# Kernel optimization log

Hardware: AMD Instinct MI355X
Metric: run time of the kernel (lower is better)

Reference implementation:

```python
import jax, jax.numpy as jnp
import numpy as np
import math

N_NODES = 100000
N_EDGES = 1600000
IN_FEATS = 64
H_FEATS = 64
NUM_CLASSES = 2
LS_D = [2, 4, 6, 8]
LS_COEFF = [1.0, 1.0, 1.0, 1.0]
K = 4  # polynomial order per conv (len of each theta)


def _chi_theta(d, coeff):
    # Faithful port of calculate_theta_Chi for d > 0: fit chi-square-like
    # density on [0,2] with a degree-3 Chebyshev series, reverse coeffs.
    n = 2 * d
    m = 1.0 / (n / 2 + 1)  # i = n/2 - 1, m = 1/(i+2)
    def y(x):
        x = np.asarray(x, dtype=np.float64)
        return 1.0 / (2 ** (n / 2) * math.gamma(n / 2)) * (x / m) ** (n / 2 - 1) * np.exp(-(x / m) / 2)
    xs = np.linspace(0.0, 2.0, 20001)
    S = np.trapz(y(xs), xs)  # dense trapezoid ~ scipy.integrate.quad on [0,2]
    lambs = np.linspace(0.0, 2.0, 500)
    c = np.polynomial.chebyshev.chebfit(lambs, y(lambs) / S, 3)
    return (c[::-1] * coeff).astype(np.float32)

THETAS_NP = np.stack([_chi_theta(d, c) for d, c in zip(LS_D, LS_COEFF)])  # [4, K]


def setup_inputs() -> dict:
    key = jax.random.key(0)
    ks = jax.random.split(key, 8)
    sc = 0.05
    return {
        "x": jax.random.normal(ks[0], (N_NODES, IN_FEATS), dtype=jnp.float32),
        "src": jax.random.randint(ks[1], (N_EDGES,), 0, N_NODES, dtype=jnp.int32),
        "dst": jax.random.randint(ks[2], (N_EDGES,), 0, N_NODES, dtype=jnp.int32),
        "thetas": jnp.asarray(THETAS_NP),
        "W1": jax.random.normal(ks[3], (IN_FEATS, H_FEATS), dtype=jnp.float32) * sc,
        "b1": jnp.zeros((H_FEATS,), dtype=jnp.float32),
        "W2": jax.random.normal(ks[4], (H_FEATS, H_FEATS), dtype=jnp.float32) * sc,
        "b2": jnp.zeros((H_FEATS,), dtype=jnp.float32),
        "Wm1": jax.random.normal(ks[5], (H_FEATS * len(LS_D), H_FEATS), dtype=jnp.float32) * sc,
        "bm1": jnp.zeros((H_FEATS,), dtype=jnp.float32),
        "Wm2": jax.random.normal(ks[6], (H_FEATS, NUM_CLASSES), dtype=jnp.float32) * sc,
        "bm2": jnp.zeros((NUM_CLASSES,), dtype=jnp.float32),
    }


def reference(x, src, dst, thetas, W1, b1, W2, b2, Wm1, bm1, Wm2, bm2):
    n = x.shape[0]
    # input MLP stem
    h = jax.nn.relu(x @ W1 + b1)
    h = jax.nn.relu(h @ W2 + b2)
    # D^{-1/2} from in-degrees (clamped to >= 1), as in DGL in_degrees()
    deg = jax.ops.segment_sum(jnp.ones_like(dst, dtype=h.dtype), dst, num_segments=n)
    dinv = jnp.maximum(deg, 1.0) ** -0.5  # [N]
    dinv = dinv[:, None]  # [N, 1]
    # shared Laplacian power sequence: feats[k] = L^k h with L = I - D^-1/2 A D^-1/2
    feats = [h]
    f = h
    for _ in range(K - 1):
        t = f * dinv                                   # [N, H]
        agg = jax.ops.segment_sum(t[src], dst, num_segments=n)  # gather-scatter SpMM
        f = f - agg * dinv
        feats.append(f)
    F = jnp.stack(feats)  # [K, N, H]
    # per-conv polynomial combination, then concat along feature dim
    h_final = jnp.einsum('ck,knh->nch', thetas, F).reshape(n, -1)  # [N, C*H]
    # output MLP (2 layers)
    h_out = jax.nn.relu(h_final @ Wm1 + bm1)
    return h_out @ Wm2 + bm2
```

## Files before the change

kernel.cpp:

```cpp
#include <hip/hip_runtime.h>
#include <math.h>

#define FS3 192
#define TS  256
#define BCAP2 4608
#define CHUNK 4096

typedef __attribute__((ext_vector_type(8))) short short8v;
typedef __attribute__((ext_vector_type(4))) float f32x4;

__device__ __forceinline__ unsigned short f2bf(float f) {
    unsigned int u = __builtin_bit_cast(unsigned int, f);
    u += 0x7fff + ((u >> 16) & 1);
    return (unsigned short)(u >> 16);
}
__device__ __forceinline__ float bf2f(unsigned short s) {
    return __builtin_bit_cast(float, ((unsigned int)s) << 16);
}
__device__ __forceinline__ void fma4(float4& a, float s, const float4& b) {
    a.x = fmaf(s, b.x, a.x);
    a.y = fmaf(s, b.y, a.y);
    a.z = fmaf(s, b.z, a.z);
    a.w = fmaf(s, b.w, a.w);
}

__global__ void zero_k(int* __restrict__ p, int n) {
    int i = blockIdx.x * blockDim.x + threadIdx.x;
    int st = gridDim.x * blockDim.x;
    for (; i < n; i += st) p[i] = 0;
}

__global__ __launch_bounds__(256) void part1_k(const int* __restrict__ src,
        const int* __restrict__ dst, int* __restrict__ gcnt,
        unsigned int* __restrict__ pairs, int E, int NB) {
    __shared__ int lcnt[512];
    __shared__ int lbase[512];
    __shared__ int lpos[512];
    int tid = threadIdx.x;
    int base = blockIdx.x * CHUNK;
    int m = E - base; if (m > CHUNK) m = CHUNK;
    for (int b = tid; b < NB; b += 256) { lcnt[b] = 0; lpos[b] = 0; }
    __syncthreads();
    for (int i = tid; i < m; i += 256)
        atomicAdd(&lcnt[dst[base + i] >> 8], 1);
    __syncthreads();
    for (int b = tid; b < NB; b += 256)
        lbase[b] = (lcnt[b] > 0) ? atomicAdd(&gcnt[b], lcnt[b]) : 0;
    __syncthreads();
    for (int i = tid; i < m; i += 256) {
        int s = src[base + i], d = dst[base + i];
        int b = d >> 8;
        int p = atomicAdd(&lpos[b], 1);
        int idx = lbase[b] + p;
        if (idx < BCAP2)
            pairs[(size_t)b * BCAP2 + idx] = (unsigned int)s | ((unsigned int)(d & 255) << 17);
    }
}

__global__ __launch_bounds__(512) void bscan_k(const int* __restrict__ gcnt,
        int* __restrict__ bbase, int* __restrict__ rowp, int NB, int E, int n) {
    __shared__ int buf[512];
    int tid = threadIdx.x;
    int v = (tid < NB) ? (gcnt[tid] > BCAP2 ? BCAP2 : gcnt[tid]) : 0;
    buf[tid] = v;
    __syncthreads();
    int x = v;
    for (int off = 1; off < 512; off <<= 1) {
        int t = (tid >= off) ? buf[tid - off] : 0;
        __syncthreads();
        x += t;
        buf[tid] = x;
        __syncthreads();
    }
    if (tid < NB) bbase[tid] = x - v;
    if (tid == 0) rowp[n] = E;
}

__global__ __launch_bounds__(256) void csr2_k(const int* __restrict__ gcnt,
        const unsigned int* __restrict__ pairs, const int* __restrict__ bbase,
        int* __restrict__ rowp, int* __restrict__ colb, float* __restrict__ dinv, int n) {
    int b = blockIdx.x;
    int tid = threadIdx.x;
    int cntb = gcnt[b]; if (cntb > BCAP2) cntb = BCAP2;
    const unsigned int* pb = pairs + (size_t)b * BCAP2;
    __shared__ int c[256];
    __shared__ int sc[256];
    __shared__ int lpos[256];
    c[tid] = 0; lpos[tid] = 0;
    __syncthreads();
    for (int i = tid; i < cntb; i += 256)
        atomicAdd(&c[pb[i] >> 17], 1);
    __syncthreads();
    int v = c[tid];
    sc[tid] = v;
    __syncthreads();
    int x = v;
    for (int off = 1; off < 256; off <<= 1) {
        int t = (tid >= off) ? sc[tid - off] : 0;
        __syncthreads();
        x += t;
        sc[tid] = x;
        __syncthreads();
    }
    int ex = x - v;
    sc[tid] = ex;
    int node = b * 256 + tid;
    if (node < n) {
        rowp[node] = bbase[b] + ex;
        dinv[node] = 1.0f / sqrtf((float)(v > 1 ? v : 1));
    }
    __syncthreads();
    for (int i = tid; i < cntb; i += 256) {
        unsigned int pk = pb[i];
        int j = pk >> 17;
        int p = atomicAdd(&lpos[j], 1);
        colb[bbase[b] + sc[j] + p] = (int)(pk & 0x1FFFF);
    }
}

__global__ __launch_bounds__(256) void mlp_k(const float* __restrict__ x,
        const float* __restrict__ W1, const float* __restrict__ b1,
        const float* __restrict__ W2, const float* __restrict__ b2,
        const float* __restrict__ dinv,
        float* __restrict__ F, unsigned short* __restrict__ Tcat, int n, int ntiles) {
    __shared__ float Ws1[64 * 64];
    __shared__ float Ws2[64 * 64];
    __shared__ float xT[64 * 68];
    int tid = threadIdx.x;
    int ti = tid >> 4, tj = tid & 15;
    for (int idx = tid; idx < 4096; idx += 256) { Ws1[idx] = W1[idx]; Ws2[idx] = W2[idx]; }
    float4 b1v = *(const float4*)&b1[4 * tj];
    float4 b2v = *(const float4*)&b2[4 * tj];

    for (int g = blockIdx.x; g < ntiles; g += gridDim.x) {
        int base = g * 64;
        __syncthreads();
        for (int it = 0; it < 4; it++) {
            int node = ti + it * 16;
            int gn = base + node;
            float4 v = make_float4(0.f, 0.f, 0.f, 0.f);
            if (gn < n) v = *(const float4*)&x[(size_t)gn * 64 + 4 * tj];
            xT[(4 * tj + 0) * 68 + node] = v.x;
            xT[(4 * tj + 1) * 68 + node] = v.y;
            xT[(4 * tj + 2) * 68 + node] = v.z;
            xT[(4 * tj + 3) * 68 + node] = v.w;
        }
        __syncthreads();

        float4 a0 = b1v, a1 = b1v, a2 = b1v, a3 = b1v;
        #pragma unroll 8
        for (int k = 0; k < 64; k++) {
            float4 xv = *(const float4*)&xT[k * 68 + 4 * ti];
            float4 wv = *(const float4*)&Ws1[k * 64 + 4 * tj];
            fma4(a0, xv.x, wv); fma4(a1, xv.y, wv); fma4(a2, xv.z, wv); fma4(a3, xv.w, wv);
        }
        __syncthreads();
        {
            int hb = (4 * tj) * 68 + 4 * ti;
            xT[hb + 0 * 68 + 0] = fmaxf(a0.x, 0.f);
            xT[hb + 1 * 68 + 0] = fmaxf(a0.y, 0.f);
            xT[hb + 2 * 68 + 0] = fmaxf(a0.z, 0.f);
            xT[hb + 3 * 68 + 0] = fmaxf(a0.w, 0.f);
            xT[hb + 0 * 68 + 1] = fmaxf(a1.x, 0.f);
            xT[hb + 1 * 68 + 1] = fmaxf(a1.y, 0.f);
            xT[hb + 2 * 68 + 1] = fmaxf(a1.z, 0.f);
            xT[hb + 3 * 68 + 1] = fmaxf(a1.w, 0.f);
            xT[hb + 0 * 68 + 2] = fmaxf(a2.x, 0.f);
            xT[hb + 1 * 68 + 2] = fmaxf(a2.y, 0.f);
            xT[hb + 2 * 68 + 2] = fmaxf(a2.z, 0.f);
            xT[hb + 3 * 68 + 2] = fmaxf(a2.w, 0.f);
            xT[hb + 0 * 68 + 3] = fmaxf(a3.x, 0.f);
            xT[hb + 1 * 68 + 3] = fmaxf(a3.y, 0.f);
            xT[hb + 2 * 68 + 3] = fmaxf(a3.z, 0.f);
            xT[hb + 3 * 68 + 3] = fmaxf(a3.w, 0.f);
        }
        __syncthreads();

        a0 = b2v; a1 = b2v; a2 = b2v; a3 = b2v;
        #pragma unroll 8
        for (int k = 0; k < 64; k++) {
            float4 xv = *(const float4*)&xT[k * 68 + 4 * ti];
            float4 wv = *(const float4*)&Ws2[k * 64 + 4 * tj];
            fma4(a0, xv.x, wv); fma4(a1, xv.y, wv); fma4(a2, xv.z, wv); fma4(a3, xv.w, wv);
        }
        int gn0 = base + 4 * ti;
#define STORE_ROW(ai, ii)                                                                  \
        {                                                                                  \
            int gn = gn0 + (ii);                                                           \
            if (gn < n) {                                                                  \
                float r0 = fmaxf(ai.x, 0.f), r1 = fmaxf(ai.y, 0.f);                        \
                float r2 = fmaxf(ai.z, 0.f), r3 = fmaxf(ai.w, 0.f);                        \
                *(float4*)&F[(size_t)gn * FS3 + 4 * tj] = make_float4(r0, r1, r2, r3);     \
                float dg = dinv[gn];                                                       \
                ushort4 tv;                                                                \
                tv.x = f2bf(r0 * dg); tv.y = f2bf(r1 * dg);                                \
                tv.z = f2bf(r2 * dg); tv.w = f2bf(r3 * dg);                                \
                *(ushort4*)&Tcat[(size_t)gn * TS + 4 * tj] = tv;                           \
            }                                                                              \
        }
        STORE_ROW(a0, 0) STORE_ROW(a1, 1) STORE_ROW(a2, 2) STORE_ROW(a3, 3)
#undef STORE_ROW
    }
}

__global__ void wm1p_k(const float* __restrict__ thetas, const float* __restrict__ Wm1,
                       unsigned short* __restrict__ Wth, unsigned short* __restrict__ Wtl) {
    int idx = blockIdx.x * blockDim.x + threadIdx.x;
    if (idx >= 16384) return;
    int j = idx & 63;
    int q = idx >> 6;
    int k = q >> 6;
    int hh = q & 63;
    float a = 0.f;
    for (int c = 0; c < 4; c++) a += thetas[c * 4 + k] * Wm1[(c * 64 + hh) * 64 + j];
    unsigned short hi = f2bf(a);
    float r = a - bf2f(hi);
    Wth[j * 256 + q] = hi;
    Wtl[j * 256 + q] = f2bf(r);
}

__global__ __launch_bounds__(256) void prop_k(const float* __restrict__ Fin,
        float* __restrict__ Fout,
        const unsigned short* __restrict__ Tin, unsigned short* __restrict__ Tout,
        const int* __restrict__ rowp, const int* __restrict__ colb,
        const float* __restrict__ dinv, int n, int writeF) {
    int w = (blockIdx.x * blockDim.x + threadIdx.x) >> 6;
    int lane = threadIdx.x & 63;
    int nA = 2 * w, nB = 2 * w + 1;
    if (nA >= n) return;
    bool hasB = (nB < n);
    int eA = rowp[nA], endA = rowp[nA + 1];
    int eB = 0, endB = 0;
    if (hasB) { eB = rowp[nB]; endB = rowp[nB + 1]; }
    float a0 = 0.f, a1 = 0.f, b0 = 0.f, b1 = 0.f;
    while (eA + 3 < endA && eB + 3 < endB) {
        int sA0 = colb[eA], sA1 = colb[eA + 1], sA2 = colb[eA + 2], sA3 = colb[eA + 3];
        int sB0 = colb[eB], sB1 = colb[eB + 1], sB2 = colb[eB + 2], sB3 = colb[eB + 3];
        float fA0 = bf2f(Tin[(size_t)sA0 * TS + lane]);
        float fA1 = bf2f(Tin[(size_t)sA1 * TS + lane]);
        float fA2 = bf2f(Tin[(size_t)sA2 * TS + lane]);
        float fA3 = bf2f(Tin[(size_t)sA3 * TS + lane]);
        float fB0 = bf2f(Tin[(size_t)sB0 * TS + lane]);
        float fB1 = bf2f(Tin[(size_t)sB1 * TS + lane]);
        float fB2 = bf2f(Tin[(size_t)sB2 * TS + lane]);
        float fB3 = bf2f(Tin[(size_t)sB3 * TS + lane]);
        a0 += fA0 + fA2; a1 += fA1 + fA3;
        b0 += fB0 + fB2; b1 += fB1 + fB3;
        eA += 4; eB += 4;
    }
    while (eA + 3 < endA) {
        int s0 = colb[eA], s1 = colb[eA + 1], s2 = colb[eA + 2], s3 = colb[eA + 3];
        float f0 = bf2f(Tin[(size_t)s0 * TS + lane]);
        float f1 = bf2f(Tin[(size_t)s1 * TS + lane]);
        float f2 = bf2f(Tin[(size_t)s2 * TS + lane]);
        float f3 = bf2f(Tin[(size_t)s3 * TS + lane]);
        a0 += f0 + f2; a1 += f1 + f3;
        eA += 4;
    }
    while (eB + 3 < endB) {
        int s0 = colb[eB], s1 = colb[eB + 1], s2 = colb[eB + 2], s3 = colb[eB + 3];
        float f0 = bf2f(Tin[(size_t)s0 * TS + lane]);
        float f1 = bf2f(Tin[(size_t)s1 * TS + lane]);
        float f2 = bf2f(Tin[(size_t)s2 * TS + lane]);
        float f3 = bf2f(Tin[(size_t)s3 * TS + lane]);
        b0 += f0 + f2; b1 += f1 + f3;
        eB += 4;
    }
    for (; eA < endA; ++eA) a0 += bf2f(Tin[(size_t)colb[eA] * TS + lane]);
    for (; eB < endB; ++eB) b0 += bf2f(Tin[(size_t)colb[eB] * TS + lane]);

    {
        float acc = a0 + a1;
        float dg = dinv[nA];
        float fo = Fin[(size_t)nA * FS3 + lane] - acc * dg;
        if (writeF) Fout[(size_t)nA * FS3 + lane] = fo;
        Tout[(size_t)nA * TS + lane] = f2bf(fo * dg);
    }
    if (hasB) {
        float acc = b0 + b1;
        float dg = dinv[nB];
        float fo = Fin[(size_t)nB * FS3 + lane] - acc * dg;
        if (writeF) Fout[(size_t)nB * FS3 + lane] = fo;
        Tout[(size_t)nB * TS + lane] = f2bf(fo * dg);
    }
}

__global__ __launch_bounds__(512, 4) void final_k(const unsigned short* __restrict__ Tcat,
        const float* __restrict__ dinv,
        const unsigned short* __restrict__ Wth, const unsigned short* __restrict__ Wtl,
        const float* __restrict__ bm1, const float* __restrict__ Wm2,
        const float* __restrict__ bm2, float* __restrict__ out, int n) {
    __shared__ float Lp[4][128][2];
    int tid = threadIdx.x;
    int w = tid >> 6, l = tid & 63;
    int cw = w & 3, half = w >> 2;
    int colg = 16 * cw + (l & 15);
    int krow = (l >> 4) * 8;

    short8v bhi[8], blo[8];
    #pragma unroll
    for (int ks = 0; ks < 8; ks++) {
        bhi[ks] = *(const short8v*)&Wth[colg * 256 + ks * 32 + krow];
        blo[ks] = *(const short8v*)&Wtl[colg * 256 + ks * 32 + krow];
    }
    float bm1c = bm1[colg];
    float w2x = Wm2[colg * 2 + 0], w2y = Wm2[colg * 2 + 1];

    int gbase = blockIdx.x * 128 + half * 64;
    const unsigned short* abase = &Tcat[(size_t)(gbase + (l & 15)) * TS + krow];

    for (int rt = 0; rt < 4; rt++) {
        f32x4 acc = {0.f, 0.f, 0.f, 0.f};
        const unsigned short* ap = abase + (size_t)rt * 16 * TS;
        #pragma unroll
        for (int ks = 0; ks < 8; ks++) {
            short8v a = *(const short8v*)(ap + ks * 32);
            acc = __builtin_amdgcn_mfma_f32_16x16x32_bf16(a, bhi[ks], acc, 0, 0, 0);
            acc = __builtin_amdgcn_mfma_f32_16x16x32_bf16(a, blo[ks], acc, 0, 0, 0);
        }
        #pragma unroll
        for (int i = 0; i < 4; i++) {
            int rl = half * 64 + rt * 16 + (l >> 4) * 4 + i;
            int grow = blockIdx.x * 128 + rl;
            float s = (grow < n) ? (1.0f / dinv[grow]) : 0.f;
            float h = fmaxf(fmaf(acc[i], s, bm1c), 0.f);
            float q0 = h * w2x, q1 = h * w2y;
            q0 += __shfl_xor(q0, 1); q1 += __shfl_xor(q1, 1);
            q0 += __shfl_xor(q0, 2); q1 += __shfl_xor(q1, 2);
            q0 += __shfl_xor(q0, 4); q1 += __shfl_xor(q1, 4);
            q0 += __shfl_xor(q0, 8); q1 += __shfl_xor(q1, 8);
            if ((l & 15) == 0) {
                Lp[cw][rl][0] = q0;
                Lp[cw][rl][1] = q1;
            }
        }
    }
    __syncthreads();
    if (tid < 256) {
        int r = tid >> 1, ch = tid & 1;
        int grow = blockIdx.x * 128 + r;
        if (grow < n) {
            float v = Lp[0][r][ch] + Lp[1][r][ch] + Lp[2][r][ch] + Lp[3][r][ch] + bm2[ch];
            out[grow * 2 + ch] = v;
        }
    }
}

extern "C" void kernel_launch(void* const* d_in, const int* in_sizes, int n_in,
                              void* d_out, int out_size, void* d_ws, size_t ws_size,
                              hipStream_t stream) {
    const float* x      = (const float*)d_in[0];
    const int*   src    = (const int*)d_in[1];
    const int*   dst    = (const int*)d_in[2];
    const float* thetas = (const float*)d_in[3];
    const float* W1     = (const float*)d_in[4];
    const float* b1     = (const float*)d_in[5];
    const float* W2     = (const float*)d_in[6];
    const float* b2     = (const float*)d_in[7];
    const float* Wm1    = (const float*)d_in[8];
    const float* bm1    = (const float*)d_in[9];
    const float* Wm2    = (const float*)d_in[10];
    const float* bm2    = (const float*)d_in[11];
    float* out = (float*)d_out;

    int n = in_sizes[0] / 64;
    int E = in_sizes[1];
    int ntiles  = (n + 63) / 64;
    int ntiles2 = (n + 127) / 128;
    int NB = (n + 255) / 256;

    float* Fbuf  = (float*)d_ws;
    float* dinv  = Fbuf + (size_t)n * FS3;
    int*   rowp  = (int*)(dinv + n);
    int*   colb  = rowp + (n + 1);
    size_t woff = (((size_t)(colb + E) - (size_t)d_ws) + 15) & ~(size_t)15;
    unsigned short* Wth = (unsigned short*)((char*)d_ws + woff);
    unsigned short* Wtl = Wth + 16384;
    int*   gcnt  = (int*)(Wtl + 16384);
    int*   bbase = gcnt + NB;
    size_t uoff = (((size_t)(bbase + NB) - (size_t)d_ws) + 255) & ~(size_t)255;
    unsigned int*   pairs = (unsigned int*)((char*)d_ws + uoff);
    unsigned short* Tcat  = (unsigned short*)pairs;

    int nchunksP = (E + CHUNK - 1) / CHUNK;

    zero_k<<<4, 256, 0, stream>>>(gcnt, NB);
    part1_k<<<nchunksP, 256, 0, stream>>>(src, dst, gcnt, pairs, E, NB);
    bscan_k<<<1, 512, 0, stream>>>(gcnt, bbase, rowp, NB, E, n);
    csr2_k<<<NB, 256, 0, stream>>>(gcnt, pairs, bbase, rowp, colb, dinv, n);

    mlp_k<<<768, 256, 0, stream>>>(x, W1, b1, W2, b2, dinv, Fbuf, Tcat, n, ntiles);
    wm1p_k<<<64, 256, 0, stream>>>(thetas, Wm1, Wth, Wtl);

    int nwaves = (n + 1) / 2;
    int pblocks = ((size_t)nwaves * 64 + 255) / 256;
    prop_k<<<pblocks, 256, 0, stream>>>(
        Fbuf + 0 * 64, Fbuf + 1 * 64, Tcat + 0 * 64, Tcat + 1 * 64, rowp, colb, dinv, n, 1);
    prop_k<<<pblocks, 256, 0, stream>>>(
        Fbuf + 1 * 64, Fbuf + 2 * 64, Tcat + 1 * 64, Tcat + 2 * 64, rowp, colb, dinv, n, 1);
    prop_k<<<pblocks, 256, 0, stream>>>(
        Fbuf + 2 * 64, Fbuf + 2 * 64, Tcat + 2 * 64, Tcat + 3 * 64, rowp, colb, dinv, n, 0);

    final_k<<<ntiles2, 512, 0, stream>>>(Tcat, dinv, Wth, Wtl, bm1, Wm2, bm2, out, n);
}
```

Baseline: 295.2 us.

## Replace fp32 residual feature buffer with bf16 hi/lo split of scaled features

```diff
diff --git a/kernel.cpp b/kernel.cpp
--- a/kernel.cpp
+++ b/kernel.cpp
@@ -1,8 +1,8 @@
 #include <hip/hip_runtime.h>
 #include <math.h>
 
-#define FS3 192
 #define TS  256
+#define GS  192
 #define BCAP2 4608
 #define CHUNK 4096
 
@@ -122,7 +122,8 @@
         const float* __restrict__ W1, const float* __restrict__ b1,
         const float* __restrict__ W2, const float* __restrict__ b2,
         const float* __restrict__ dinv,
-        float* __restrict__ F, unsigned short* __restrict__ Tcat, int n, int ntiles) {
+        unsigned short* __restrict__ Ghi, unsigned short* __restrict__ Glo,
+        int n, int ntiles) {
     __shared__ float Ws1[64 * 64];
     __shared__ float Ws2[64 * 64];
     __shared__ float xT[64 * 68];
@@ -188,14 +189,16 @@
         {                                                                                  \
             int gn = gn0 + (ii);                                                           \
             if (gn < n) {                                                                  \
-                float r0 = fmaxf(ai.x, 0.f), r1 = fmaxf(ai.y, 0.f);                        \
-                float r2 = fmaxf(ai.z, 0.f), r3 = fmaxf(ai.w, 0.f);                        \
-                *(float4*)&F[(size_t)gn * FS3 + 4 * tj] = make_float4(r0, r1, r2, r3);     \
                 float dg = dinv[gn];                                                       \
-                ushort4 tv;                                                                \
-                tv.x = f2bf(r0 * dg); tv.y = f2bf(r1 * dg);                                \
-                tv.z = f2bf(r2 * dg); tv.w = f2bf(r3 * dg);                                \
-                *(ushort4*)&Tcat[(size_t)gn * TS + 4 * tj] = tv;                           \
+                float g0 = fmaxf(ai.x, 0.f) * dg, g1 = fmaxf(ai.y, 0.f) * dg;              \
+                float g2 = fmaxf(ai.z, 0.f) * dg, g3 = fmaxf(ai.w, 0.f) * dg;              \
+                ushort4 hv, lv;                                                            \
+                hv.x = f2bf(g0); lv.x = f2bf(g0 - bf2f(hv.x));                             \
+                hv.y = f2bf(g1); lv.y = f2bf(g1 - bf2f(hv.y));                             \
+                hv.z = f2bf(g2); lv.z = f2bf(g2 - bf2f(hv.z));                             \
+                hv.w = f2bf(g3); lv.w = f2bf(g3 - bf2f(hv.w));                             \
+                *(ushort4*)&Ghi[(size_t)gn * TS + 4 * tj] = hv;                            \
+                *(ushort4*)&Glo[(size_t)gn * GS + 4 * tj] = lv;                            \
             }                                                                              \
         }
         STORE_ROW(a0, 0) STORE_ROW(a1, 1) STORE_ROW(a2, 2) STORE_ROW(a3, 3)
@@ -219,11 +222,13 @@
     Wtl[j * 256 + q] = f2bf(r);
 }
 
-__global__ __launch_bounds__(256) void prop_k(const float* __restrict__ Fin,
-        float* __restrict__ Fout,
-        const unsigned short* __restrict__ Tin, unsigned short* __restrict__ Tout,
+__global__ __launch_bounds__(256) void prop_k(
+        const unsigned short* __restrict__ TinHi,
+        const unsigned short* __restrict__ TinLo,
+        unsigned short* __restrict__ ToutHi,
+        unsigned short* __restrict__ ToutLo,
         const int* __restrict__ rowp, const int* __restrict__ colb,
-        const float* __restrict__ dinv, int n, int writeF) {
+        const float* __restrict__ dinv, int n, int writeLo) {
     int w = (blockIdx.x * blockDim.x + threadIdx.x) >> 6;
     int lane = threadIdx.x & 63;
     int nA = 2 * w, nB = 2 * w + 1;
@@ -233,55 +238,93 @@
     int eB = 0, endB = 0;
     if (hasB) { eB = rowp[nB]; endB = rowp[nB + 1]; }
     float a0 = 0.f, a1 = 0.f, b0 = 0.f, b1 = 0.f;
-    while (eA + 3 < endA && eB + 3 < endB) {
-        int sA0 = colb[eA], sA1 = colb[eA + 1], sA2 = colb[eA + 2], sA3 = colb[eA + 3];
-        int sB0 = colb[eB], sB1 = colb[eB + 1], sB2 = colb[eB + 2], sB3 = colb[eB + 3];
-        float fA0 = bf2f(Tin[(size_t)sA0 * TS + lane]);
-        float fA1 = bf2f(Tin[(size_t)sA1 * TS + lane]);
-        float fA2 = bf2f(Tin[(size_t)sA2 * TS + lane]);
-        float fA3 = bf2f(Tin[(size_t)sA3 * TS + lane]);
-        float fB0 = bf2f(Tin[(size_t)sB0 * TS + lane]);
-        float fB1 = bf2f(Tin[(size_t)sB1 * TS + lane]);
-        float fB2 = bf2f(Tin[(size_t)sB2 * TS + lane]);
-        float fB3 = bf2f(Tin[(size_t)sB3 * TS + lane]);
-        a0 += fA0 + fA2; a1 += fA1 + fA3;
-        b0 += fB0 + fB2; b1 += fB1 + fB3;
-        eA += 4; eB += 4;
+    while (eA + 7 < endA && eB + 7 < endB) {
+        int sA0 = __builtin_nontemporal_load(&colb[eA]);
+        int sA1 = __builtin_nontemporal_load(&colb[eA + 1]);
+        int sA2 = __builtin_nontemporal_load(&colb[eA + 2]);
+        int sA3 = __builtin_nontemporal_load(&colb[eA + 3]);
+        int sA4 = __builtin_nontemporal_load(&colb[eA + 4]);
+        int sA5 = __builtin_nontemporal_load(&colb[eA + 5]);
+        int sA6 = __builtin_nontemporal_load(&colb[eA + 6]);
+        int sA7 = __builtin_nontemporal_load(&colb[eA + 7]);
+        int sB0 = __builtin_nontemporal_load(&colb[eB]);
+        int sB1 = __builtin_nontemporal_load(&colb[eB + 1]);
+        int sB2 = __builtin_nontemporal_load(&colb[eB + 2]);
+        int sB3 = __builtin_nontemporal_load(&colb[eB + 3]);
+        int sB4 = __builtin_nontemporal_load(&colb[eB + 4]);
+        int sB5 = __builtin_nontemporal_load(&colb[eB + 5]);
+        int sB6 = __builtin_nontemporal_load(&colb[eB + 6]);
+        int sB7 = __builtin_nontemporal_load(&colb[eB + 7]);
+        float fA0 = bf2f(TinHi[(size_t)sA0 * TS + lane]);
+        float fA1 = bf2f(TinHi[(size_t)sA1 * TS + lane]);
+        float fA2 = bf2f(TinHi[(size_t)sA2 * TS + lane]);
+        float fA3 = bf2f(TinHi[(size_t)sA3 * TS + lane]);
+        float fA4 = bf2f(TinHi[(size_t)sA4 * TS + lane]);
+        float fA5 = bf2f(TinHi[(size_t)sA5 * TS + lane]);
+        float fA6 = bf2f(TinHi[(size_t)sA6 * TS + lane]);
+        float fA7 = bf2f(TinHi[(size_t)sA7 * TS + lane]);
+        float fB0 = bf2f(TinHi[(size_t)sB0 * TS + lane]);
+        float fB1 = bf2f(TinHi[(size_t)sB1 * TS + lane]);
+        float fB2 = bf2f(TinHi[(size_t)sB2 * TS + lane]);
+        float fB3 = bf2f(TinHi[(size_t)sB3 * TS + lane]);
+        float fB4 = bf2f(TinHi[(size_t)sB4 * TS + lane]);
+        float fB5 = bf2f(TinHi[(size_t)sB5 * TS + lane]);
+        float fB6 = bf2f(TinHi[(size_t)sB6 * TS + lane]);
+        float fB7 = bf2f(TinHi[(size_t)sB7 * TS + lane]);
+        a0 += (fA0 + fA2) + (fA4 + fA6);
+        a1 += (fA1 + fA3) + (fA5 + fA7);
+        b0 += (fB0 + fB2) + (fB4 + fB6);
+        b1 += (fB1 + fB3) + (fB5 + fB7);
+        eA += 8; eB += 8;
     }
     while (eA + 3 < endA) {
-        int s0 = colb[eA], s1 = colb[eA + 1], s2 = colb[eA + 2], s3 = colb[eA + 3];
-        float f0 = bf2f(Tin[(size_t)s0 * TS + lane]);
-        float f1 = bf2f(Tin[(size_t)s1 * TS + lane]);
-        float f2 = bf2f(Tin[(size_t)s2 * TS + lane]);
-        float f3 = bf2f(Tin[(size_t)s3 * TS + lane]);
+        int s0 = __builtin_nontemporal_load(&colb[eA]);
+        int s1 = __builtin_nontemporal_load(&colb[eA + 1]);
+        int s2 = __builtin_nontemporal_load(&colb[eA + 2]);
+        int s3 = __builtin_nontemporal_load(&colb[eA + 3]);
+        float f0 = bf2f(TinHi[(size_t)s0 * TS + lane]);
+        float f1 = bf2f(TinHi[(size_t)s1 * TS + lane]);
+        float f2 = bf2f(TinHi[(size_t)s2 * TS + lane]);
+        float f3 = bf2f(TinHi[(size_t)s3 * TS + lane]);
         a0 += f0 + f2; a1 += f1 + f3;
         eA += 4;
     }
     while (eB + 3 < endB) {
-        int s0 = colb[eB], s1 = colb[eB + 1], s2 = colb[eB + 2], s3 = colb[eB + 3];
-        float f0 = bf2f(Tin[(size_t)s0 * TS + lane]);
-        float f1 = bf2f(Tin[(size_t)s1 * TS + lane]);
-        float f2 = bf2f(Tin[(size_t)s2 * TS + lane]);
-        float f3 = bf2f(Tin[(size_t)s3 * TS + lane]);
+        int s0 = __builtin_nontemporal_load(&colb[eB]);
+        int s1 = __builtin_nontemporal_load(&colb[eB + 1]);
+        int s2 = __builtin_nontemporal_load(&colb[eB + 2]);
+        int s3 = __builtin_nontemporal_load(&colb[eB + 3]);
+        float f0 = bf2f(TinHi[(size_t)s0 * TS + lane]);
+        float f1 = bf2f(TinHi[(size_t)s1 * TS + lane]);
+        float f2 = bf2f(TinHi[(size_t)s2 * TS + lane]);
+        float f3 = bf2f(TinHi[(size_t)s3 * TS + lane]);
         b0 += f0 + f2; b1 += f1 + f3;
         eB += 4;
     }
-    for (; eA < endA; ++eA) a0 += bf2f(Tin[(size_t)colb[eA] * TS + lane]);
-    for (; eB < endB; ++eB) b0 += bf2f(Tin[(size_t)colb[eB] * TS + lane]);
+    for (; eA < endA; ++eA) a0 += bf2f(TinHi[(size_t)__builtin_nontemporal_load(&colb[eA]) * TS + lane]);
+    for (; eB < endB; ++eB) b0 += bf2f(TinHi[(size_t)__builtin_nontemporal_load(&colb[eB]) * TS + lane]);
 
     {
         float acc = a0 + a1;
         float dg = dinv[nA];
-        float fo = Fin[(size_t)nA * FS3 + lane] - acc * dg;
-        if (writeF) Fout[(size_t)nA * FS3 + lane] = fo;
-        Tout[(size_t)nA * TS + lane] = f2bf(fo * dg);
+        float gin = bf2f(__builtin_nontemporal_load(&TinHi[(size_t)nA * TS + lane]))
+                  + bf2f(__builtin_nontemporal_load(&TinLo[(size_t)nA * GS + lane]));
+        float go = gin - dg * dg * acc;
+        unsigned short hi = f2bf(go);
+        ToutHi[(size_t)nA * TS + lane] = hi;
+        if (writeLo)
+            __builtin_nontemporal_store(f2bf(go - bf2f(hi)), &ToutLo[(size_t)nA * GS + lane]);
     }
     if (hasB) {
         float acc = b0 + b1;
         float dg = dinv[nB];
-        float fo = Fin[(size_t)nB * FS3 + lane] - acc * dg;
-        if (writeF) Fout[(size_t)nB * FS3 + lane] = fo;
-        Tout[(size_t)nB * TS + lane] = f2bf(fo * dg);
+        float gin = bf2f(__builtin_nontemporal_load(&TinHi[(size_t)nB * TS + lane]))
+                  + bf2f(__builtin_nontemporal_load(&TinLo[(size_t)nB * GS + lane]));
+        float go = gin - dg * dg * acc;
+        unsigned short hi = f2bf(go);
+        ToutHi[(size_t)nB * TS + lane] = hi;
+        if (writeLo)
+            __builtin_nontemporal_store(f2bf(go - bf2f(hi)), &ToutLo[(size_t)nB * GS + lane]);
     }
 }
 
@@ -369,8 +412,8 @@
     int ntiles2 = (n + 127) / 128;
     int NB = (n + 255) / 256;
 
-    float* Fbuf  = (float*)d_ws;
-    float* dinv  = Fbuf + (size_t)n * FS3;
+    unsigned short* Glo = (unsigned short*)d_ws;
+    float* dinv  = (float*)(Glo + (size_t)n * GS);
     int*   rowp  = (int*)(dinv + n);
     int*   colb  = rowp + (n + 1);
     size_t woff = (((size_t)(colb + E) - (size_t)d_ws) + 15) & ~(size_t)15;
@@ -380,7 +423,7 @@
     int*   bbase = gcnt + NB;
     size_t uoff = (((size_t)(bbase + NB) - (size_t)d_ws) + 255) & ~(size_t)255;
     unsigned int*   pairs = (unsigned int*)((char*)d_ws + uoff);
-    unsigned short* Tcat  = (unsigned short*)pairs;
+    unsigned short* Ghi   = (unsigned short*)pairs;
 
     int nchunksP = (E + CHUNK - 1) / CHUNK;
 
@@ -389,17 +432,17 @@
     bscan_k<<<1, 512, 0, stream>>>(gcnt, bbase, rowp, NB, E, n);
     csr2_k<<<NB, 256, 0, stream>>>(gcnt, pairs, bbase, rowp, colb, dinv, n);
 
-    mlp_k<<<768, 256, 0, stream>>>(x, W1, b1, W2, b2, dinv, Fbuf, Tcat, n, ntiles);
+    mlp_k<<<768, 256, 0, stream>>>(x, W1, b1, W2, b2, dinv, Ghi, Glo, n, ntiles);
     wm1p_k<<<64, 256, 0, stream>>>(thetas, Wm1, Wth, Wtl);
 
     int nwaves = (n + 1) / 2;
     int pblocks = ((size_t)nwaves * 64 + 255) / 256;
     prop_k<<<pblocks, 256, 0, stream>>>(
-        Fbuf + 0 * 64, Fbuf + 1 * 64, Tcat + 0 * 64, Tcat + 1 * 64, rowp, colb, dinv, n, 1);
+        Ghi + 0 * 64, Glo + 0 * 64, Ghi + 1 * 64, Glo + 1 * 64, rowp, colb, dinv, n, 1);
     prop_k<<<pblocks, 256, 0, stream>>>(
-        Fbuf + 1 * 64, Fbuf + 2 * 64, Tcat + 1 * 64, Tcat + 2 * 64, rowp, colb, dinv, n, 1);
+        Ghi + 1 * 64, Glo + 1 * 64, Ghi + 2 * 64, Glo + 2 * 64, rowp, colb, dinv, n, 1);
     prop_k<<<pblocks, 256, 0, stream>>>(
-        Fbuf + 2 * 64, Fbuf + 2 * 64, Tcat + 2 * 64, Tcat + 3 * 64, rowp, colb, dinv, n, 0);
-
-    final_k<<<ntiles2, 512, 0, stream>>>(Tcat, dinv, Wth, Wtl, bm1, Wm2, bm2, out, n);
-}
+        Ghi + 2 * 64, Glo + 2 * 64, Ghi + 3 * 64, Glo + 2 * 64, rowp, colb, dinv, n, 0);
+
+    final_k<<<ntiles2, 512, 0, stream>>>(Ghi, dinv, Wth, Wtl, bm1, Wm2, bm2, out, n);
+}
```

After: 341.2 us. 15.6% more time.

## Store propagated features as 8-column bf16 hi/lo slabs for cache-local gathers

Applied to the files above, without the earlier changes.

```diff
diff --git a/kernel.cpp b/kernel.cpp
--- a/kernel.cpp
+++ b/kernel.cpp
@@ -1,13 +1,13 @@
 #include <hip/hip_runtime.h>
 #include <math.h>
 
-#define FS3 192
-#define TS  256
 #define BCAP2 4608
 #define CHUNK 4096
+#define NPB 256
 
 typedef __attribute__((ext_vector_type(8))) short short8v;
 typedef __attribute__((ext_vector_type(4))) float f32x4;
+
 
 __device__ __forceinline__ unsigned short f2bf(float f) {
     unsigned int u = __builtin_bit_cast(unsigned int, f);
@@ -122,7 +122,8 @@
         const float* __restrict__ W1, const float* __restrict__ b1,
         const float* __restrict__ W2, const float* __restrict__ b2,
         const float* __restrict__ dinv,
-        float* __restrict__ F, unsigned short* __restrict__ Tcat, int n, int ntiles) {
+        unsigned short* __restrict__ Ghi, unsigned short* __restrict__ Glo,
+        int n, int ntiles, size_t npad8) {
     __shared__ float Ws1[64 * 64];
     __shared__ float Ws2[64 * 64];
     __shared__ float xT[64 * 68];
@@ -131,6 +132,8 @@
     for (int idx = tid; idx < 4096; idx += 256) { Ws1[idx] = W1[idx]; Ws2[idx] = W2[idx]; }
     float4 b1v = *(const float4*)&b1[4 * tj];
     float4 b2v = *(const float4*)&b2[4 * tj];
+    int kb = tj >> 1;
+    int off = (tj & 1) * 4;
 
     for (int g = blockIdx.x; g < ntiles; g += gridDim.x) {
         int base = g * 64;
@@ -188,14 +191,16 @@
         {                                                                                  \
             int gn = gn0 + (ii);                                                           \
             if (gn < n) {                                                                  \
-                float r0 = fmaxf(ai.x, 0.f), r1 = fmaxf(ai.y, 0.f);                        \
-                float r2 = fmaxf(ai.z, 0.f), r3 = fmaxf(ai.w, 0.f);                        \
-                *(float4*)&F[(size_t)gn * FS3 + 4 * tj] = make_float4(r0, r1, r2, r3);     \
                 float dg = dinv[gn];                                                       \
-                ushort4 tv;                                                                \
-                tv.x = f2bf(r0 * dg); tv.y = f2bf(r1 * dg);                                \
-                tv.z = f2bf(r2 * dg); tv.w = f2bf(r3 * dg);                                \
-                *(ushort4*)&Tcat[(size_t)gn * TS + 4 * tj] = tv;                           \
+                float g0 = fmaxf(ai.x, 0.f) * dg, g1 = fmaxf(ai.y, 0.f) * dg;              \
+                float g2 = fmaxf(ai.z, 0.f) * dg, g3 = fmaxf(ai.w, 0.f) * dg;              \
+                ushort4 hv, lv;                                                            \
+                hv.x = f2bf(g0); lv.x = f2bf(g0 - bf2f(hv.x));                             \
+                hv.y = f2bf(g1); lv.y = f2bf(g1 - bf2f(hv.y));                             \
+                hv.z = f2bf(g2); lv.z = f2bf(g2 - bf2f(hv.z));                             \
+                hv.w = f2bf(g3); lv.w = f2bf(g3 - bf2f(hv.w));                             \
+                *(ushort4*)&Ghi[(size_t)kb * npad8 + (size_t)gn * 8 + off] = hv;           \
+                *(ushort4*)&Glo[(size_t)kb * npad8 + (size_t)gn * 8 + off] = lv;           \
             }                                                                              \
         }
         STORE_ROW(a0, 0) STORE_ROW(a1, 1) STORE_ROW(a2, 2) STORE_ROW(a3, 3)
@@ -219,83 +224,61 @@
     Wtl[j * 256 + q] = f2bf(r);
 }
 
-__global__ __launch_bounds__(256) void prop_k(const float* __restrict__ Fin,
-        float* __restrict__ Fout,
-        const unsigned short* __restrict__ Tin, unsigned short* __restrict__ Tout,
+__global__ __launch_bounds__(256) void prop_k(
+        const unsigned short* __restrict__ GhiSlabIn,
+        const unsigned short* __restrict__ GloSlabIn,
+        unsigned short* __restrict__ GhiSlabOut,
+        unsigned short* __restrict__ GloSlabOut,
         const int* __restrict__ rowp, const int* __restrict__ colb,
-        const float* __restrict__ dinv, int n, int writeF) {
-    int w = (blockIdx.x * blockDim.x + threadIdx.x) >> 6;
+        const float* __restrict__ dinv, int n, size_t npad8, int writeLo) {
+    int cb = blockIdx.x & 7;
+    int grp = blockIdx.x >> 3;
+    const unsigned short* Gin = GhiSlabIn + (size_t)cb * npad8;
+    const unsigned short* Lin = GloSlabIn + (size_t)cb * npad8;
+    unsigned short* Hout = GhiSlabOut + (size_t)cb * npad8;
+    unsigned short* Lout = GloSlabOut + (size_t)cb * npad8;
     int lane = threadIdx.x & 63;
-    int nA = 2 * w, nB = 2 * w + 1;
-    if (nA >= n) return;
-    bool hasB = (nB < n);
-    int eA = rowp[nA], endA = rowp[nA + 1];
-    int eB = 0, endB = 0;
-    if (hasB) { eB = rowp[nB]; endB = rowp[nB + 1]; }
-    float a0 = 0.f, a1 = 0.f, b0 = 0.f, b1 = 0.f;
-    while (eA + 3 < endA && eB + 3 < endB) {
-        int sA0 = colb[eA], sA1 = colb[eA + 1], sA2 = colb[eA + 2], sA3 = colb[eA + 3];
-        int sB0 = colb[eB], sB1 = colb[eB + 1], sB2 = colb[eB + 2], sB3 = colb[eB + 3];
-        float fA0 = bf2f(Tin[(size_t)sA0 * TS + lane]);
-        float fA1 = bf2f(Tin[(size_t)sA1 * TS + lane]);
-        float fA2 = bf2f(Tin[(size_t)sA2 * TS + lane]);
-        float fA3 = bf2f(Tin[(size_t)sA3 * TS + lane]);
-        float fB0 = bf2f(Tin[(size_t)sB0 * TS + lane]);
-        float fB1 = bf2f(Tin[(size_t)sB1 * TS + lane]);
-        float fB2 = bf2f(Tin[(size_t)sB2 * TS + lane]);
-        float fB3 = bf2f(Tin[(size_t)sB3 * TS + lane]);
-        a0 += fA0 + fA2; a1 += fA1 + fA3;
-        b0 += fB0 + fB2; b1 += fB1 + fB3;
-        eA += 4; eB += 4;
-    }
-    while (eA + 3 < endA) {
-        int s0 = colb[eA], s1 = colb[eA + 1], s2 = colb[eA + 2], s3 = colb[eA + 3];
-        float f0 = bf2f(Tin[(size_t)s0 * TS + lane]);
-        float f1 = bf2f(Tin[(size_t)s1 * TS + lane]);
-        float f2 = bf2f(Tin[(size_t)s2 * TS + lane]);
-        float f3 = bf2f(Tin[(size_t)s3 * TS + lane]);
-        a0 += f0 + f2; a1 += f1 + f3;
-        eA += 4;
-    }
-    while (eB + 3 < endB) {
-        int s0 = colb[eB], s1 = colb[eB + 1], s2 = colb[eB + 2], s3 = colb[eB + 3];
-        float f0 = bf2f(Tin[(size_t)s0 * TS + lane]);
-        float f1 = bf2f(Tin[(size_t)s1 * TS + lane]);
-        float f2 = bf2f(Tin[(size_t)s2 * TS + lane]);
-        float f3 = bf2f(Tin[(size_t)s3 * TS + lane]);
-        b0 += f0 + f2; b1 += f1 + f3;
-        eB += 4;
-    }
-    for (; eA < endA; ++eA) a0 += bf2f(Tin[(size_t)colb[eA] * TS + lane]);
-    for (; eB < endB; ++eB) b0 += bf2f(Tin[(size_t)colb[eB] * TS + lane]);
-
-    {
-        float acc = a0 + a1;
-        float dg = dinv[nA];
-        float fo = Fin[(size_t)nA * FS3 + lane] - acc * dg;
-        if (writeF) Fout[(size_t)nA * FS3 + lane] = fo;
-        Tout[(size_t)nA * TS + lane] = f2bf(fo * dg);
-    }
-    if (hasB) {
-        float acc = b0 + b1;
-        float dg = dinv[nB];
-        float fo = Fin[(size_t)nB * FS3 + lane] - acc * dg;
-        if (writeF) Fout[(size_t)nB * FS3 + lane] = fo;
-        Tout[(size_t)nB * TS + lane] = f2bf(fo * dg);
-    }
-}
-
-__global__ __launch_bounds__(512, 4) void final_k(const unsigned short* __restrict__ Tcat,
+    int wv = threadIdx.x >> 6;
+    int c = lane & 7, es = lane >> 3;
+    int nb = grp * NPB;
+    int ne = nb + NPB; if (ne > n) ne = n;
+    for (int nd = nb + wv; nd < ne; nd += 4) {
+        int beg = rowp[nd], end = rowp[nd + 1];
+        float acc = 0.f;
+        int e = beg + es;
+        for (; e + 8 < end; e += 16) {
+            int s0 = colb[e], s1 = colb[e + 8];
+            float f0 = bf2f(Gin[(size_t)s0 * 8 + c]);
+            float f1 = bf2f(Gin[(size_t)s1 * 8 + c]);
+            acc += f0 + f1;
+        }
+        if (e < end) acc += bf2f(Gin[(size_t)colb[e] * 8 + c]);
+        acc += __shfl_xor(acc, 8);
+        acc += __shfl_xor(acc, 16);
+        acc += __shfl_xor(acc, 32);
+        if (es == 0) {
+            float dg = dinv[nd];
+            float gown = bf2f(Gin[(size_t)nd * 8 + c]) + bf2f(Lin[(size_t)nd * 8 + c]);
+            float go = gown - dg * dg * acc;
+            unsigned short hi = f2bf(go);
+            Hout[(size_t)nd * 8 + c] = hi;
+            if (writeLo) Lout[(size_t)nd * 8 + c] = f2bf(go - bf2f(hi));
+        }
+    }
+}
+
+__global__ __launch_bounds__(512, 4) void final_k(const unsigned short* __restrict__ Ghi,
         const float* __restrict__ dinv,
         const unsigned short* __restrict__ Wth, const unsigned short* __restrict__ Wtl,
         const float* __restrict__ bm1, const float* __restrict__ Wm2,
-        const float* __restrict__ bm2, float* __restrict__ out, int n) {
+        const float* __restrict__ bm2, float* __restrict__ out, int n, size_t npad8) {
     __shared__ float Lp[4][128][2];
     int tid = threadIdx.x;
     int w = tid >> 6, l = tid & 63;
     int cw = w & 3, half = w >> 2;
     int colg = 16 * cw + (l & 15);
     int krow = (l >> 4) * 8;
+    int rgrp = l >> 4;
 
     short8v bhi[8], blo[8];
     #pragma unroll
@@ -306,15 +289,13 @@
     float bm1c = bm1[colg];
     float w2x = Wm2[colg * 2 + 0], w2y = Wm2[colg * 2 + 1];
 
-    int gbase = blockIdx.x * 128 + half * 64;
-    const unsigned short* abase = &Tcat[(size_t)(gbase + (l & 15)) * TS + krow];
-
     for (int rt = 0; rt < 4; rt++) {
+        int r = blockIdx.x * 128 + half * 64 + rt * 16 + (l & 15);
+        size_t rbase = (size_t)rgrp * npad8 + (size_t)r * 8;
         f32x4 acc = {0.f, 0.f, 0.f, 0.f};
-        const unsigned short* ap = abase + (size_t)rt * 16 * TS;
         #pragma unroll
         for (int ks = 0; ks < 8; ks++) {
-            short8v a = *(const short8v*)(ap + ks * 32);
+            short8v a = *(const short8v*)&Ghi[rbase + (size_t)(ks * 4) * npad8];
             acc = __builtin_amdgcn_mfma_f32_16x16x32_bf16(a, bhi[ks], acc, 0, 0, 0);
             acc = __builtin_amdgcn_mfma_f32_16x16x32_bf16(a, blo[ks], acc, 0, 0, 0);
         }
@@ -367,10 +348,12 @@
     int E = in_sizes[1];
     int ntiles  = (n + 63) / 64;
     int ntiles2 = (n + 127) / 128;
+    int npad = ntiles2 * 128;
+    size_t npad8 = (size_t)npad * 8;
     int NB = (n + 255) / 256;
 
-    float* Fbuf  = (float*)d_ws;
-    float* dinv  = Fbuf + (size_t)n * FS3;
+    unsigned short* Glo = (unsigned short*)d_ws;
+    float* dinv  = (float*)(Glo + 24 * npad8);
     int*   rowp  = (int*)(dinv + n);
     int*   colb  = rowp + (n + 1);
     size_t woff = (((size_t)(colb + E) - (size_t)d_ws) + 15) & ~(size_t)15;
@@ -380,7 +363,7 @@
     int*   bbase = gcnt + NB;
     size_t uoff = (((size_t)(bbase + NB) - (size_t)d_ws) + 255) & ~(size_t)255;
     unsigned int*   pairs = (unsigned int*)((char*)d_ws + uoff);
-    unsigned short* Tcat  = (unsigned short*)pairs;
+    unsigned short* Ghi   = (unsigned short*)pairs;
 
     int nchunksP = (E + CHUNK - 1) / CHUNK;
 
@@ -389,17 +372,19 @@
     bscan_k<<<1, 512, 0, stream>>>(gcnt, bbase, rowp, NB, E, n);
     csr2_k<<<NB, 256, 0, stream>>>(gcnt, pairs, bbase, rowp, colb, dinv, n);
 
-    mlp_k<<<768, 256, 0, stream>>>(x, W1, b1, W2, b2, dinv, Fbuf, Tcat, n, ntiles);
+    mlp_k<<<768, 256, 0, stream>>>(x, W1, b1, W2, b2, dinv, Ghi, Glo, n, ntiles, npad8);
     wm1p_k<<<64, 256, 0, stream>>>(thetas, Wm1, Wth, Wtl);
 
-    int nwaves = (n + 1) / 2;
-    int pblocks = ((size_t)nwaves * 64 + 255) / 256;
-    prop_k<<<pblocks, 256, 0, stream>>>(
-        Fbuf + 0 * 64, Fbuf + 1 * 64, Tcat + 0 * 64, Tcat + 1 * 64, rowp, colb, dinv, n, 1);
-    prop_k<<<pblocks, 256, 0, stream>>>(
-        Fbuf + 1 * 64, Fbuf + 2 * 64, Tcat + 1 * 64, Tcat + 2 * 64, rowp, colb, dinv, n, 1);
-    prop_k<<<pblocks, 256, 0, stream>>>(
-        Fbuf + 2 * 64, Fbuf + 2 * 64, Tcat + 2 * 64, Tcat + 3 * 64, rowp, colb, dinv, n, 0);
-
-    final_k<<<ntiles2, 512, 0, stream>>>(Tcat, dinv, Wth, Wtl, bm1, Wm2, bm2, out, n);
-}
+    int pgrid = ((n + NPB - 1) / NPB) * 8;
+    prop_k<<<pgrid, 256, 0, stream>>>(
+        Ghi + 0 * npad8, Glo + 0 * npad8, Ghi + 8 * npad8, Glo + 8 * npad8,
+        rowp, colb, dinv, n, npad8, 1);
+    prop_k<<<pgrid, 256, 0, stream>>>(
+        Ghi + 8 * npad8, Glo + 8 * npad8, Ghi + 16 * npad8, Glo + 16 * npad8,
+        rowp, colb, dinv, n, npad8, 1);
+    prop_k<<<pgrid, 256, 0, stream>>>(
+        Ghi + 16 * npad8, Glo + 16 * npad8, Ghi + 24 * npad8, Glo,
+        rowp, colb, dinv, n, npad8, 0);
+
+    final_k<<<ntiles2, 512, 0, stream>>>(Ghi, dinv, Wth, Wtl, bm1, Wm2, bm2, out, n, npad8);
+}
```

Result: slower. 799.4 us (+170.8%).
